# Optimization experiments

Hardware: AMD Instinct MI355X
Metric: run time of the kernel (lower is better)

Reference implementation:

```python
import jax, jax.numpy as jnp
import numpy as np

D_MODEL = 2048
N_HEAD = 32
N_KV_HEAD = 8
N_REP = N_HEAD // N_KV_HEAD
D_K = D_MODEL // N_HEAD
THETA = 10000.0
B, S = 2, 1024


def setup_inputs() -> dict:
    key = jax.random.key(0)
    ks = jax.random.split(key, 9)
    sd = 1.0 / np.sqrt(D_MODEL)
    return {
        "x": jax.random.normal(ks[0], (B, S, D_MODEL), jnp.float32),
        "Wq": jax.random.normal(ks[1], (D_MODEL, D_MODEL), jnp.float32) * sd,
        "bq": jax.random.normal(ks[2], (D_MODEL,), jnp.float32) * 0.02,
        "Wk": jax.random.normal(ks[3], (D_MODEL, N_KV_HEAD * D_K), jnp.float32) * sd,
        "bk": jax.random.normal(ks[4], (N_KV_HEAD * D_K,), jnp.float32) * 0.02,
        "Wv": jax.random.normal(ks[5], (D_MODEL, N_KV_HEAD * D_K), jnp.float32) * sd,
        "bv": jax.random.normal(ks[6], (N_KV_HEAD * D_K,), jnp.float32) * 0.02,
        "Wo": jax.random.normal(ks[7], (D_MODEL, D_MODEL), jnp.float32) * sd,
        "bo": jax.random.normal(ks[8], (D_MODEL,), jnp.float32) * 0.02,
    }


def _apply_rope(t, pos):
    # t: [b, h, s, d_k], pos: [s]
    half = D_K // 2
    inv_freq = 1.0 / (THETA ** (jnp.arange(half, dtype=jnp.float32) * 2.0 / D_K))
    ang = pos[:, None].astype(jnp.float32) * inv_freq[None, :]  # [s, half]
    cos = jnp.cos(ang)[None, None]  # [1,1,s,half]
    sin = jnp.sin(ang)[None, None]
    te = t[..., 0::2]
    to = t[..., 1::2]
    re = te * cos - to * sin
    ro = te * sin + to * cos
    return jnp.stack([re, ro], axis=-1).reshape(t.shape)


def reference(x, Wq, bq, Wk, bk, Wv, bv, Wo, bo):
    b, s, _ = x.shape
    q = (x @ Wq + bq).reshape(b, s, N_HEAD, D_K).transpose(0, 2, 1, 3)
    k = (x @ Wk + bk).reshape(b, s, N_KV_HEAD, D_K).transpose(0, 2, 1, 3)
    v = (x @ Wv + bv).reshape(b, s, N_KV_HEAD, D_K).transpose(0, 2, 1, 3)
    pos = jnp.arange(s)
    q = _apply_rope(q, pos)
    k = _apply_rope(k, pos)
    # GQA head repeat: [b, n_kv, s, d] -> [b, n_head, s, d]
    k = jnp.repeat(k, N_REP, axis=1)
    v = jnp.repeat(v, N_REP, axis=1)
    scores = jnp.einsum('bhnd,bhmd->bhnm', q, k) / jnp.sqrt(jnp.float32(D_K))
    mask = jnp.tril(jnp.ones((s, s), dtype=bool))
    scores = jnp.where(mask[None, None], scores, jnp.float32(-jnp.inf))
    probs = jax.nn.softmax(scores, axis=-1)
    out = jnp.einsum('bhnm,bhmd->bhnd', probs, v)
    out = out.transpose(0, 2, 1, 3).reshape(b, s, D_MODEL)
    return out @ Wo + bo
```

## Files before the change

kernel.cpp:

```cpp
#include <hip/hip_runtime.h>
#include <hip/hip_bf16.h>

#define D_MODEL 2048
#define N_HEAD 32
#define N_KV_HEAD 8
#define N_REP 4
#define D_K 64
#define S_LEN 1024
#define B_SZ 2
#define M_ROWS (B_SZ * S_LEN)
#define KV_DIM (N_KV_HEAD * D_K)
#define QKV_N 3072
#define KOFF 2048
#define VOFF 2560
#define LOG2E 1.44269504088896f
#define TAB_N (S_LEN * 32)

typedef __attribute__((ext_vector_type(8))) short short8;
typedef __attribute__((ext_vector_type(4))) float f32x4;
typedef __attribute__((ext_vector_type(16))) float f32x16;

#define EXP2F(x) __builtin_amdgcn_exp2f(x)

__device__ inline unsigned short f2bf(float f) {
    union { float f; unsigned int u; } x{f};
    unsigned int r = x.u + 0x7fffu + ((x.u >> 16) & 1u);
    return (unsigned short)(r >> 16);
}
__device__ inline float bf2f(unsigned short b) {
    union { unsigned int u; float f; } x; x.u = ((unsigned int)b) << 16; return x.f;
}
__device__ inline void store_c(float* p, float v) { *p = v; }
__device__ inline void store_c(unsigned short* p, float v) { *p = f2bf(v); }

__device__ inline void load_lds16(const unsigned short* g, unsigned short* l) {
    __builtin_amdgcn_global_load_lds(
        (const __attribute__((address_space(1))) unsigned int*)g,
        (__attribute__((address_space(3))) unsigned int*)l, 16, 0, 0);
}

__device__ __forceinline__ unsigned int permpack(float hi_f, float lo_f) {
    union { float f; unsigned int u; } a{hi_f}, b{lo_f};
    return __builtin_amdgcn_perm(a.u, b.u, 0x07060302u);
}

__global__ __launch_bounds__(256) void prep_kernel(
        const float* __restrict__ x,
        const float* __restrict__ Wq_, const float* __restrict__ Wk_,
        const float* __restrict__ Wv_, const float* __restrict__ Wo_,
        unsigned short* __restrict__ xbf,
        unsigned short* __restrict__ WtQKV, unsigned short* __restrict__ WtO) {
    const int z = blockIdx.z;
    if (z >= 4) {
        int idx = ((z - 4) * 1024 + blockIdx.y * 32 + blockIdx.x) * 256 + threadIdx.x;
#pragma unroll
        for (int half = 0; half < 2; half++) {
            int i = idx + half * 524288;
            float4 v = ((const float4*)x)[i];
            unsigned int lo = (unsigned int)f2bf(v.x) | ((unsigned int)f2bf(v.y) << 16);
            unsigned int hi = (unsigned int)f2bf(v.z) | ((unsigned int)f2bf(v.w) << 16);
            ((uint2*)xbf)[i] = make_uint2(lo, hi);
        }
        return;
    }
    const float* src; unsigned short* dst; int N;
    switch (z) {
        case 0: src = Wq_; dst = WtQKV; N = D_MODEL; break;
        case 1: src = Wk_; dst = WtQKV + (size_t)KOFF * D_MODEL; N = KV_DIM; break;
        case 2: src = Wv_; dst = WtQKV + (size_t)VOFF * D_MODEL; N = KV_DIM; break;
        default: src = Wo_; dst = WtO; N = D_MODEL; break;
    }
    int n0 = blockIdx.x * 64;
    if (n0 >= N) return;
    int k0 = blockIdx.y * 64;
    int t = threadIdx.x;
    int n = n0 + (t >> 2);
    int ks = k0 + (t & 3) * 16;
    unsigned int pk[8];
#pragma unroll
    for (int i = 0; i < 8; i++) {
        float a = src[(size_t)(ks + 2 * i) * N + n];
        float b = src[(size_t)(ks + 2 * i + 1) * N + n];
        pk[i] = (unsigned int)f2bf(a) | ((unsigned int)f2bf(b) << 16);
    }
    uint4* d = (uint4*)&dst[(size_t)n * D_MODEL + ks];
    d[0] = make_uint4(pk[0], pk[1], pk[2], pk[3]);
    d[1] = make_uint4(pk[4], pk[5], pk[6], pk[7]);
}

__global__ void prep_small_kernel(const float* __restrict__ bq, const float* __restrict__ bk,
                                  const float* __restrict__ bv, float* __restrict__ dst,
                                  float2* __restrict__ tab) {
    int i = blockIdx.x * blockDim.x + threadIdx.x;
    if (i < QKV_N) {
        dst[i] = (i < KOFF) ? bq[i] : (i < VOFF) ? bk[i - KOFF] : bv[i - VOFF];
    }
    int j = i - QKV_N;
    if (j >= 0 && j < TAB_N) {
        int s = j >> 5, p = j & 31;
        float invf = EXP2F((float)p * -0.41524101186f);
        float ang = (float)s * invf;
        tab[j] = make_float2(__cosf(ang), __sinf(ang));
    }
}

template <typename TC, bool ROPE>
__global__ __launch_bounds__(256) void gemm_bf16_kernel(
        const unsigned short* __restrict__ A,
        const unsigned short* __restrict__ Bt,
        const float* __restrict__ bias,
        const float2* __restrict__ rtab,
        TC* __restrict__ C, int M, int N, int K) {
    __shared__ unsigned short As[128 * 64];
    __shared__ unsigned short Bs[64 * 64];
    const int tid = threadIdx.x, lane = tid & 63;
    const int w = tid >> 6, wm = w >> 1, wn = w & 1;
    const int quad = lane >> 4, lr = lane & 15;
    const int bm = blockIdx.y * 128, bn = blockIdx.x * 64;

    f32x4 acc[4][2];
#pragma unroll
    for (int i = 0; i < 4; i++)
#pragma unroll
        for (int j = 0; j < 2; j++) acc[i][j] = (f32x4){0.f, 0.f, 0.f, 0.f};

    for (int k0 = 0; k0 < K; k0 += 64) {
        __syncthreads();
#pragma unroll
        for (int it = 0; it < 4; it++) {
            int slot = it * 256 + tid;
            int row = slot >> 3;
            int qc = (slot & 7) ^ (row & 7);
            load_lds16(A + (size_t)(bm + row) * K + k0 + qc * 8, &As[slot * 8]);
        }
#pragma unroll
        for (int it = 0; it < 2; it++) {
            int slot = it * 256 + tid;
            int row = slot >> 3;
            int qc = (slot & 7) ^ (row & 7);
            load_lds16(Bt + (size_t)(bn + row) * K + k0 + qc * 8, &Bs[slot * 8]);
        }
        __syncthreads();
#pragma unroll
        for (int ks = 0; ks < 2; ks++) {
            short8 af[4], bf[2];
#pragma unroll
            for (int i = 0; i < 4; i++) {
                int row = wm * 64 + i * 16 + lr;
                af[i] = *(const short8*)&As[(row * 8 + ((ks * 4 + quad) ^ (lr & 7))) * 8];
            }
#pragma unroll
            for (int j = 0; j < 2; j++) {
                int row = wn * 32 + j * 16 + lr;
                bf[j] = *(const short8*)&Bs[(row * 8 + ((ks * 4 + quad) ^ (lr & 7))) * 8];
            }
#pragma unroll
            for (int i = 0; i < 4; i++)
#pragma unroll
                for (int j = 0; j < 2; j++)
                    acc[i][j] = __builtin_amdgcn_mfma_f32_16x16x32_bf16(af[i], bf[j], acc[i][j], 0, 0, 0);
        }
    }
#pragma unroll
    for (int i = 0; i < 4; i++) {
#pragma unroll
        for (int j = 0; j < 2; j++) {
            int col = bn + wn * 32 + j * 16 + lr;
            int row0 = bm + wm * 64 + i * 16 + quad * 4;
            float bj = bias[col];
            if constexpr (ROPE) {
                bool isv = col >= VOFF;
                bool isq = col < KOFF;
                int ip = (col & 63) >> 1;
                bool even = !(lr & 1);
#pragma unroll
                for (int r = 0; r < 4; r++) {
                    float v = acc[i][j][r] + bj;
                    float pv = __shfl_xor(v, 1);
                    float outv = v;
                    if (!isv) {
                        int s = (row0 + r) & (S_LEN - 1);
                        float2 cs = rtab[s * 32 + ip];
                        outv = v * cs.x + (even ? -pv : pv) * cs.y;
                        if (isq) outv *= 0.125f * LOG2E;
                    }
                    store_c(&C[(size_t)(row0 + r) * N + col], outv);
                }
            } else {
#pragma unroll
                for (int r = 0; r < 4; r++)
                    store_c(&C[(size_t)(row0 + r) * N + col], acc[i][j][r] + bj);
            }
        }
    }
}

#define AST 72
#define RESCALE_THR 8.0f
struct Pre { uint4 k0, k1, v0, v1; };

__device__ __forceinline__ void issue_pre(const unsigned short* kb,
                                          const unsigned short* vb,
                                          int j0, int tid, Pre& p) {
    int f0 = tid, f1 = tid + 256;
    p.k0 = *(const uint4*)(kb + (size_t)(j0 + (f0 >> 3)) * QKV_N + (f0 & 7) * 8);
    p.k1 = *(const uint4*)(kb + (size_t)(j0 + (f1 >> 3)) * QKV_N + (f1 & 7) * 8);
    int kp = tid & 31, dg = tid >> 5;
    p.v0 = *(const uint4*)(vb + (size_t)(j0 + 2 * kp) * QKV_N + dg * 8);
    p.v1 = *(const uint4*)(vb + (size_t)(j0 + 2 * kp + 1) * QKV_N + dg * 8);
}
__device__ __forceinline__ void commit_pre(unsigned short* Ks, unsigned short* Vt,
                                           int tid, const Pre& p) {
    int f0 = tid, f1 = tid + 256;
    *(uint4*)&Ks[(f0 >> 3) * AST + (f0 & 7) * 8] = p.k0;
    *(uint4*)&Ks[(f1 >> 3) * AST + (f1 & 7) * 8] = p.k1;
    int kp = tid & 31, dg = tid >> 5;
    const unsigned short* ta = (const unsigned short*)&p.v0;
    const unsigned short* tb = (const unsigned short*)&p.v1;
#pragma unroll
    for (int i = 0; i < 8; i++) {
        unsigned int pk = (unsigned int)ta[i] | ((unsigned int)tb[i] << 16);
        *(unsigned int*)&Vt[(dg * 8 + i) * AST + 2 * kp] = pk;
    }
}

__global__ __launch_bounds__(256) void attn_mfma_kernel(
        const unsigned short* __restrict__ qkv,
        unsigned short* __restrict__ obf) {
    __shared__ unsigned short SM[4 * 64 * AST];
    const int tid = threadIdx.x;
    const int w = tid >> 6, lane = tid & 63;
    const int lq = lane & 31, hi = lane >> 5;
    const int hi8 = hi * 8, hi4 = hi * 4;
    const int h = blockIdx.y, b = blockIdx.z;
    const int kvh = h >> 2;
    const unsigned short* kb = qkv + (size_t)(b * S_LEN) * QKV_N + KOFF + kvh * D_K;
    const unsigned short* vb = qkv + (size_t)(b * S_LEN) * QKV_N + VOFF + kvh * D_K;

    const int qt = b ? 7 - (int)blockIdx.x : (int)blockIdx.x;
    const int nt = 2 * qt + 2;
    const int qw0 = qt * 128 + w * 32;
    const int qg = qw0 + lq;

    short8 aq[4];
    {
        const unsigned short* qp = qkv + (size_t)(b * S_LEN + qg) * QKV_N + h * D_K + hi8;
#pragma unroll
        for (int st = 0; st < 4; st++) aq[st] = *(const short8*)(qp + st * 16);
    }
    f32x16 oacc[2];
#pragma unroll
    for (int dt = 0; dt < 2; dt++)
#pragma unroll
        for (int r = 0; r < 16; r++) oacc[dt][r] = 0.f;
    float m = -1e30f, l = 0.f;

    Pre pre;
    issue_pre(kb, vb, 0, tid, pre);
    commit_pre(SM, SM + 64 * AST, tid, pre);
    if (nt > 1) issue_pre(kb, vb, 64, tid, pre);
    __syncthreads();

    for (int t = 0; t < nt; t++) {
        const int par = t & 1;
        unsigned short* Ks = SM + par * (2 * 64 * AST);
        unsigned short* Vt = Ks + 64 * AST;
        const int t64 = t * 64;
        if (t64 <= qw0 + 31) {
            f32x16 s0, s1;
#pragma unroll
            for (int r = 0; r < 16; r++) { s0[r] = 0.f; s1[r] = 0.f; }
            __builtin_amdgcn_s_setprio(1);
#pragma unroll
            for (int st = 0; st < 4; st++) {
                short8 k0 = *(const short8*)&Ks[lq * AST + st * 16 + hi8];
                short8 k1 = *(const short8*)&Ks[(32 + lq) * AST + st * 16 + hi8];
                s0 = __builtin_amdgcn_mfma_f32_32x32x16_bf16(k0, aq[st], s0, 0, 0, 0);
                s1 = __builtin_amdgcn_mfma_f32_32x32x16_bf16(k1, aq[st], s1, 0, 0, 0);
            }
            __builtin_amdgcn_s_setprio(0);
            float px[32];
#pragma unroll
            for (int r = 0; r < 16; r++) { px[r] = s0[r]; px[16 + r] = s1[r]; }
            if (t64 + 63 > qw0) {
#pragma unroll
                for (int kh = 0; kh < 2; kh++)
#pragma unroll
                    for (int r = 0; r < 16; r++) {
                        int kg = t64 + kh * 32 + ((r & 3) + 8 * (r >> 2)) + hi4;
                        if (kg > qg) px[kh * 16 + r] = -1e30f;
                    }
            }
            float tm[16];
#pragma unroll
            for (int i = 0; i < 16; i++) tm[i] = fmaxf(px[i], px[i + 16]);
#pragma unroll
            for (int i = 0; i < 8; i++) tm[i] = fmaxf(tm[i], tm[i + 8]);
#pragma unroll
            for (int i = 0; i < 4; i++) tm[i] = fmaxf(tm[i], tm[i + 4]);
            float lmax = fmaxf(fmaxf(tm[0], tm[1]), fmaxf(tm[2], tm[3]));
            union { float f; unsigned int u; } mb{lmax};
            auto rr = __builtin_amdgcn_permlane32_swap((int)mb.u, (int)mb.u, false, false);
            union { unsigned int u; float f; } ra, rb;
            ra.u = (unsigned int)rr[0];
            rb.u = (unsigned int)rr[1];
            float mn = fmaxf(m, fmaxf(ra.f, rb.f));
            if (!__all(mn - m <= RESCALE_THR)) {
                float corr = EXP2F(m - mn);
                m = mn;
                l *= corr;
#pragma unroll
                for (int dt = 0; dt < 2; dt++)
#pragma unroll
                    for (int r = 0; r < 16; r++) oacc[dt][r] *= corr;
            }
            float p[32], pm[32];
#pragma unroll
            for (int i = 0; i < 32; i++) {
                p[i] = EXP2F(px[i] - m);
                union { float f; unsigned int u; } pu{p[i]};
                pu.u &= 0xFFFF0000u;
                pm[i] = pu.f;
            }
            float ts[16];
#pragma unroll
            for (int i = 0; i < 16; i++) ts[i] = pm[i] + pm[i + 16];
#pragma unroll
            for (int i = 0; i < 8; i++) ts[i] = ts[i] + ts[i + 8];
#pragma unroll
            for (int i = 0; i < 4; i++) ts[i] = ts[i] + ts[i + 4];
            float lsum = (ts[0] + ts[1]) + (ts[2] + ts[3]);
            union { float f; unsigned int u; } sb{lsum};
            auto rr2 = __builtin_amdgcn_permlane32_swap((int)sb.u, (int)sb.u, false, false);
            union { unsigned int u; float f; } sa2, sb2;
            sa2.u = (unsigned int)rr2[0];
            sb2.u = (unsigned int)rr2[1];
            l = l + (sa2.f + sb2.f);
            short8 pf[4];
#pragma unroll
            for (int kh = 0; kh < 2; kh++)
#pragma unroll
                for (int s = 0; s < 2; s++) {
                    int base = kh * 16 + 8 * s;
                    unsigned int a01 = permpack(p[base + 1], p[base + 0]);
                    unsigned int a23 = permpack(p[base + 3], p[base + 2]);
                    unsigned int a45 = permpack(p[base + 5], p[base + 4]);
                    unsigned int a67 = permpack(p[base + 7], p[base + 6]);
                    auto r02 = __builtin_amdgcn_permlane32_swap((int)a01, (int)a45, false, false);
                    auto r13 = __builtin_amdgcn_permlane32_swap((int)a23, (int)a67, false, false);
                    union { unsigned int wd[4]; short8 v; } pk;
                    pk.wd[0] = (unsigned int)r02[0];
                    pk.wd[1] = (unsigned int)r13[0];
                    pk.wd[2] = (unsigned int)r02[1];
                    pk.wd[3] = (unsigned int)r13[1];
                    pf[kh * 2 + s] = pk.v;
                }
            __builtin_amdgcn_s_setprio(1);
#pragma unroll
            for (int dt = 0; dt < 2; dt++)
#pragma unroll
                for (int sl = 0; sl < 4; sl++) {
                    short8 va = *(const short8*)&Vt[(dt * 32 + lq) * AST + sl * 16 + hi8];
                    oacc[dt] = __builtin_amdgcn_mfma_f32_32x32x16_bf16(va, pf[sl], oacc[dt], 0, 0, 0);
                }
            __builtin_amdgcn_s_setprio(0);
        }
        if (t + 1 < nt) {
            unsigned short* Kn = SM + (par ^ 1) * (2 * 64 * AST);
            commit_pre(Kn, Kn + 64 * AST, tid, pre);
            if (t + 2 < nt) issue_pre(kb, vb, (t + 2) * 64, tid, pre);
        }
        __syncthreads();
    }
    float inv = 1.f / l;
    unsigned short* Os = SM + w * 32 * AST;
#pragma unroll
    for (int dt = 0; dt < 2; dt++)
#pragma unroll
        for (int j = 0; j < 8; j++) {
            int d = dt * 32 + ((2 * j) & 3) + 8 * (j >> 1) + hi4;
            unsigned int pk = (unsigned int)f2bf(oacc[dt][2 * j] * inv)
                            | ((unsigned int)f2bf(oacc[dt][2 * j + 1] * inv) << 16);
            *(unsigned int*)&Os[lq * AST + d] = pk;
        }
    __syncthreads();
#pragma unroll
    for (int j = 0; j < 4; j++) {
        int row = j * 8 + (lane >> 3);
        short8 v = *(const short8*)&Os[row * AST + (lane & 7) * 8];
        int qrow = b * S_LEN + qw0 + row;
        *(short8*)&obf[(size_t)qrow * D_MODEL + h * D_K + (lane & 7) * 8] = v;
    }
}

extern "C" void kernel_launch(void* const* d_in, const int* in_sizes, int n_in,
                              void* d_out, int out_size, void* d_ws, size_t ws_size,
                              hipStream_t stream) {
    const float* x  = (const float*)d_in[0];
    const float* Wq = (const float*)d_in[1];
    const float* bq = (const float*)d_in[2];
    const float* Wk = (const float*)d_in[3];
    const float* bk = (const float*)d_in[4];
    const float* Wv = (const float*)d_in[5];
    const float* bv = (const float*)d_in[6];
    const float* Wo = (const float*)d_in[7];
    const float* bo = (const float*)d_in[8];
    float* out = (float*)d_out;

    unsigned short* xbf   = (unsigned short*)d_ws;
    unsigned short* WtQKV = xbf + (size_t)M_ROWS * D_MODEL;
    unsigned short* WtO   = WtQKV + (size_t)QKV_N * D_MODEL;
    unsigned short* qkv   = WtO + (size_t)D_MODEL * D_MODEL;
    float* bias_qkv       = (float*)(qkv + (size_t)M_ROWS * QKV_N);
    float2* rtab          = (float2*)(bias_qkv + QKV_N);
    unsigned short* obf   = xbf;

    dim3 gb(256);

    prep_kernel<<<dim3(32, 32, 6), gb, 0, stream>>>(x, Wq, Wk, Wv, Wo, xbf, WtQKV, WtO);
    prep_small_kernel<<<(QKV_N + TAB_N + 255) / 256, gb, 0, stream>>>(bq, bk, bv, bias_qkv, rtab);
    gemm_bf16_kernel<unsigned short, true><<<dim3(QKV_N / 64, M_ROWS / 128), gb, 0, stream>>>(
        xbf, WtQKV, bias_qkv, rtab, qkv, M_ROWS, QKV_N, D_MODEL);
    attn_mfma_kernel<<<dim3(8, N_HEAD, B_SZ), gb, 0, stream>>>(qkv, obf);
    gemm_bf16_kernel<float, false><<<dim3(D_MODEL / 64, M_ROWS / 128), gb, 0, stream>>>(
        obf, WtO, bo, nullptr, out, M_ROWS, D_MODEL, D_MODEL);
}
```

Before: 218.9 us.

## Double-buffer GEMM LDS tiles and fold bias/RoPE table prep into prep kernel

The bf16 GEMM now keeps two LDS buffers for the A and B tiles and issues the global-to-LDS loads for the next K step before computing on the current one. This drops one barrier per iteration and lets memory latency overlap the MFMA work. The small kernel that builds the bias and the RoPE table is merged into the prep kernel as an extra z-slice, which removes one launch. The cost is twice the LDS per block, which may reduce occupancy. There is also a possible race, because the async direct-to-LDS load for the next stage is not waited on by an explicit vmcnt before the barrier.

```diff
diff --git a/kernel.cpp b/kernel.cpp
--- a/kernel.cpp
+++ b/kernel.cpp
@@ -48,9 +48,26 @@
         const float* __restrict__ x,
         const float* __restrict__ Wq_, const float* __restrict__ Wk_,
         const float* __restrict__ Wv_, const float* __restrict__ Wo_,
+        const float* __restrict__ bq, const float* __restrict__ bk,
+        const float* __restrict__ bv,
         unsigned short* __restrict__ xbf,
-        unsigned short* __restrict__ WtQKV, unsigned short* __restrict__ WtO) {
+        unsigned short* __restrict__ WtQKV, unsigned short* __restrict__ WtO,
+        float* __restrict__ bias_qkv, float2* __restrict__ rtab) {
     const int z = blockIdx.z;
+    if (z == 6) {
+        int i = (blockIdx.y * 32 + blockIdx.x) * 256 + threadIdx.x;
+        if (i < QKV_N) {
+            bias_qkv[i] = (i < KOFF) ? bq[i] : (i < VOFF) ? bk[i - KOFF] : bv[i - VOFF];
+        }
+        int j = i - QKV_N;
+        if (j >= 0 && j < TAB_N) {
+            int s = j >> 5, p = j & 31;
+            float invf = EXP2F((float)p * -0.41524101186f);
+            float ang = (float)s * invf;
+            rtab[j] = make_float2(__cosf(ang), __sinf(ang));
+        }
+        return;
+    }
     if (z >= 4) {
         int idx = ((z - 4) * 1024 + blockIdx.y * 32 + blockIdx.x) * 256 + threadIdx.x;
 #pragma unroll
@@ -88,22 +105,6 @@
     d[1] = make_uint4(pk[4], pk[5], pk[6], pk[7]);
 }
 
-__global__ void prep_small_kernel(const float* __restrict__ bq, const float* __restrict__ bk,
-                                  const float* __restrict__ bv, float* __restrict__ dst,
-                                  float2* __restrict__ tab) {
-    int i = blockIdx.x * blockDim.x + threadIdx.x;
-    if (i < QKV_N) {
-        dst[i] = (i < KOFF) ? bq[i] : (i < VOFF) ? bk[i - KOFF] : bv[i - VOFF];
-    }
-    int j = i - QKV_N;
-    if (j >= 0 && j < TAB_N) {
-        int s = j >> 5, p = j & 31;
-        float invf = EXP2F((float)p * -0.41524101186f);
-        float ang = (float)s * invf;
-        tab[j] = make_float2(__cosf(ang), __sinf(ang));
-    }
-}
-
 template <typename TC, bool ROPE>
 __global__ __launch_bounds__(256) void gemm_bf16_kernel(
         const unsigned short* __restrict__ A,
@@ -111,8 +112,8 @@
         const float* __restrict__ bias,
         const float2* __restrict__ rtab,
         TC* __restrict__ C, int M, int N, int K) {
-    __shared__ unsigned short As[128 * 64];
-    __shared__ unsigned short Bs[64 * 64];
+    __shared__ unsigned short As[2][128 * 64];
+    __shared__ unsigned short Bs[2][64 * 64];
     const int tid = threadIdx.x, lane = tid & 63;
     const int w = tid >> 6, wm = w >> 1, wn = w & 1;
     const int quad = lane >> 4, lr = lane & 15;
@@ -124,35 +125,40 @@
 #pragma unroll
         for (int j = 0; j < 2; j++) acc[i][j] = (f32x4){0.f, 0.f, 0.f, 0.f};
 
-    for (int k0 = 0; k0 < K; k0 += 64) {
-        __syncthreads();
+    auto stage = [&](int buf, int k0) {
 #pragma unroll
         for (int it = 0; it < 4; it++) {
             int slot = it * 256 + tid;
             int row = slot >> 3;
             int qc = (slot & 7) ^ (row & 7);
-            load_lds16(A + (size_t)(bm + row) * K + k0 + qc * 8, &As[slot * 8]);
+            load_lds16(A + (size_t)(bm + row) * K + k0 + qc * 8, &As[buf][slot * 8]);
         }
 #pragma unroll
         for (int it = 0; it < 2; it++) {
             int slot = it * 256 + tid;
             int row = slot >> 3;
             int qc = (slot & 7) ^ (row & 7);
-            load_lds16(Bt + (size_t)(bn + row) * K + k0 + qc * 8, &Bs[slot * 8]);
-        }
-        __syncthreads();
+            load_lds16(Bt + (size_t)(bn + row) * K + k0 + qc * 8, &Bs[buf][slot * 8]);
+        }
+    };
+
+    stage(0, 0);
+    __syncthreads();
+    int cur = 0;
+    for (int k0 = 0; k0 < K; k0 += 64) {
+        if (k0 + 64 < K) stage(cur ^ 1, k0 + 64);
 #pragma unroll
         for (int ks = 0; ks < 2; ks++) {
             short8 af[4], bf[2];
 #pragma unroll
             for (int i = 0; i < 4; i++) {
                 int row = wm * 64 + i * 16 + lr;
-                af[i] = *(const short8*)&As[(row * 8 + ((ks * 4 + quad) ^ (lr & 7))) * 8];
+                af[i] = *(const short8*)&As[cur][(row * 8 + ((ks * 4 + quad) ^ (lr & 7))) * 8];
             }
 #pragma unroll
             for (int j = 0; j < 2; j++) {
                 int row = wn * 32 + j * 16 + lr;
-                bf[j] = *(const short8*)&Bs[(row * 8 + ((ks * 4 + quad) ^ (lr & 7))) * 8];
+                bf[j] = *(const short8*)&Bs[cur][(row * 8 + ((ks * 4 + quad) ^ (lr & 7))) * 8];
             }
 #pragma unroll
             for (int i = 0; i < 4; i++)
@@ -160,6 +166,8 @@
                 for (int j = 0; j < 2; j++)
                     acc[i][j] = __builtin_amdgcn_mfma_f32_16x16x32_bf16(af[i], bf[j], acc[i][j], 0, 0, 0);
         }
+        __syncthreads();
+        cur ^= 1;
     }
 #pragma unroll
     for (int i = 0; i < 4; i++) {
@@ -417,8 +425,8 @@
 
     dim3 gb(256);
 
-    prep_kernel<<<dim3(32, 32, 6), gb, 0, stream>>>(x, Wq, Wk, Wv, Wo, xbf, WtQKV, WtO);
-    prep_small_kernel<<<(QKV_N + TAB_N + 255) / 256, gb, 0, stream>>>(bq, bk, bv, bias_qkv, rtab);
+    prep_kernel<<<dim3(32, 32, 7), gb, 0, stream>>>(x, Wq, Wk, Wv, Wo, bq, bk, bv,
+                                                    xbf, WtQKV, WtO, bias_qkv, rtab);
     gemm_bf16_kernel<unsigned short, true><<<dim3(QKV_N / 64, M_ROWS / 128), gb, 0, stream>>>(
         xbf, WtQKV, bias_qkv, rtab, qkv, M_ROWS, QKV_N, D_MODEL);
     attn_mfma_kernel<<<dim3(8, N_HEAD, B_SZ), gb, 0, stream>>>(qkv, obf);
```

Result: faster. 214.4 us (-2.1%).
